# Kernel tuning notes

Hardware: AMD Instinct MI355X
Metric: run time of the kernel (lower is better)

## Reference

```python
import jax, jax.numpy as jnp
import numpy as np

N, Fdim, Aout = 8192, 32, 8
AVG_DEG = 32.0  # target average degree for the random graph


def setup_inputs() -> dict:
    key = jax.random.key(0)
    ks = jax.random.split(key, 12)
    x = jax.random.normal(ks[0], (N, Fdim), dtype=jnp.float32)
    # binary adjacency, zero diagonal (GCNConv adds self-loops itself)
    u = jax.random.uniform(ks[1], (N, N), dtype=jnp.float32)
    adj = (u < (AVG_DEG / N)).astype(jnp.float32)
    adj = adj * (1.0 - jnp.eye(N, dtype=jnp.float32))
    mask = (jax.random.uniform(ks[2], (N,), dtype=jnp.float32) < 0.5).astype(jnp.float32)

    def lin(k, fout, fin):
        s = 1.0 / np.sqrt(fin)
        return jax.random.uniform(k, (fout, fin), jnp.float32, -s, s)

    return {
        "x": x, "adj": adj, "mask": mask,
        "w1": lin(ks[3], 64, Fdim), "b1": jnp.zeros((64,), jnp.float32),
        "w2": lin(ks[4], 128, 64), "b2": jnp.zeros((128,), jnp.float32),
        "wg": lin(ks[5], 128, 128), "bg": jnp.zeros((128,), jnp.float32),
        "wd": lin(ks[6], 128, 128), "bd": jnp.zeros((128,), jnp.float32),
        "wp1": lin(ks[7], 128, 256), "bp1": jnp.zeros((128,), jnp.float32),
        "wp2": lin(ks[8], 64, 128), "bp2": jnp.zeros((64,), jnp.float32),
        "wo": lin(ks[9], Aout, 64), "bo": jnp.zeros((Aout,), jnp.float32),
    }


def reference(x, adj, mask, w1, b1, w2, b2, wg, bg, wd, bd, wp1, bp1, wp2, bp2, wo, bo):
    # encoder MLP
    h = jax.nn.relu(x @ w1.T + b1)           # [N,64]
    h = jax.nn.relu(h @ w2.T + b2)           # [N,128]
    # GCNConv with default self-loops and symmetric normalization:
    # out = D^{-1/2} (A + I) D^{-1/2} (h W^T) + b
    a_hat = adj + jnp.eye(adj.shape[0], dtype=adj.dtype)
    deg = jnp.sum(a_hat, axis=1)             # >= 1 thanks to self-loops
    dinv = jax.lax.rsqrt(deg)
    msg = h @ wg.T                            # [N,128]
    agg = dinv[:, None] * (a_hat @ (dinv[:, None] * msg))  # normalized aggregation
    g = jax.nn.relu(agg + bg)
    g = jax.nn.relu(g @ wd.T + bd)
    f = jnp.concatenate([g, h], axis=1)       # [N,256]
    p = jax.nn.relu(f @ wp1.T + bp1)
    p = jax.nn.relu(p @ wp2.T + bp2)
    out = (p @ wo.T + bo) * mask[:, None]     # [N,Aout]
    return out
```

## Files before the change

kernel.cpp:

```cpp
#include <hip/hip_runtime.h>

#define N_NODES 8192
#define CAP 128
#define ETILE 16
#define DTILE 8
constexpr int AST = 132;
constexpr int WST = 129;

typedef unsigned u32x4 __attribute__((ext_vector_type(4)));

__global__ __launch_bounds__(256, 4) void scan_kernel(
    const float* __restrict__ adj, int* __restrict__ cnt,
    int* __restrict__ nbr) {
  const int t = threadIdx.x;
  const int lane = t & 63;
  const int row = blockIdx.x * 4 + (t >> 6);
  const u32x4* rowp = (const u32x4*)(adj + (size_t)row * N_NODES);
  u32x4 v[8], vn[8];
#pragma unroll
  for (int i = 0; i < 8; ++i) v[i] = __builtin_nontemporal_load(&rowp[i * 64 + lane]);
  int running = 0;
  int* nbr_row = nbr + (size_t)row * CAP;
  for (int ch = 0; ch < 4; ++ch) {
    if (ch < 3) {
      const u32x4* cp = rowp + (ch + 1) * 512;
#pragma unroll
      for (int i = 0; i < 8; ++i) vn[i] = __builtin_nontemporal_load(&cp[i * 64 + lane]);
    }
    int c = 0;
#pragma unroll
    for (int i = 0; i < 8; ++i)
      c += (v[i].x != 0u) + (v[i].y != 0u) + (v[i].z != 0u) + (v[i].w != 0u);
    int incl = c;
#pragma unroll
    for (int s = 1; s < 64; s <<= 1) {
      int n = __shfl_up(incl, s);
      if (lane >= s) incl += n;
    }
    int off = running + incl - c;
    running += __shfl(incl, 63);
    const int colbase = ch * 2048;
#pragma unroll
    for (int i = 0; i < 8; ++i) {
      if (v[i].x | v[i].y | v[i].z | v[i].w) {
        const int col = colbase + (i * 64 + lane) * 4;
        if (v[i].x) { if (off < CAP) nbr_row[off] = col + 0; ++off; }
        if (v[i].y) { if (off < CAP) nbr_row[off] = col + 1; ++off; }
        if (v[i].z) { if (off < CAP) nbr_row[off] = col + 2; ++off; }
        if (v[i].w) { if (off < CAP) nbr_row[off] = col + 3; ++off; }
      }
    }
#pragma unroll
    for (int i = 0; i < 8; ++i) v[i] = vn[i];
  }
  if (lane == 0) cnt[row] = running;
}

template <int TILE, int K, int KSPLIT, int F, bool RELU, bool BIAS, int SCALEMODE>
__device__ __forceinline__ void layer_op(
    const float (*__restrict__ A0)[AST], const float (*__restrict__ A1)[AST],
    float (*__restrict__ Aout)[AST], float (*__restrict__ Wb)[WST],
    const float* __restrict__ W, const float* __restrict__ bias,
    float* __restrict__ gout, const float* __restrict__ rowscale,
    const int* __restrict__ degcnt, int n0, int t) {
  constexpr int KC = 32;
  constexpr int NCH = K / KC;
  constexpr int ACT = (F * TILE < 256) ? F * TILE : 256;
  constexpr int RS = ACT / F;
  constexpr int RPT = TILE / RS;
  const int c = t % F;
  const int rb = t / F;
  float acc[RPT];
#pragma unroll
  for (int i = 0; i < RPT; ++i) acc[i] = 0.f;

  for (int ch = 0; ch < NCH; ++ch) {
#pragma unroll
    for (int i = 0; i < (F * KC + 255) / 256; ++i) {
      int lin = t + i * 256;
      if ((F * KC) % 256 == 0 || lin < F * KC) {
        int k = lin % KC, f = lin / KC;
        Wb[k][f] = W[(size_t)f * K + ch * KC + k];
      }
    }
    __syncthreads();
    if (t < ACT) {
      const float (*__restrict__ As)[AST] = (ch * KC < KSPLIT) ? A0 : A1;
      const int kb = (ch * KC < KSPLIT) ? ch * KC : ch * KC - KSPLIT;
#pragma unroll
      for (int kg = 0; kg < KC / 4; ++kg) {
        float w0 = Wb[kg * 4 + 0][c];
        float w1v = Wb[kg * 4 + 1][c];
        float w2v = Wb[kg * 4 + 2][c];
        float w3v = Wb[kg * 4 + 3][c];
#pragma unroll
        for (int i = 0; i < RPT; ++i) {
          const float4 a = *(const float4*)&As[rb + i * RS][kb + kg * 4];
          acc[i] = fmaf(a.x, w0, acc[i]);
          acc[i] = fmaf(a.y, w1v, acc[i]);
          acc[i] = fmaf(a.z, w2v, acc[i]);
          acc[i] = fmaf(a.w, w3v, acc[i]);
        }
      }
    }
    __syncthreads();
  }
  if (t < ACT) {
#pragma unroll
    for (int i = 0; i < RPT; ++i) {
      float v = acc[i];
      if (BIAS) v += bias[c];
      if (RELU) v = fmaxf(v, 0.f);
      int node = n0 + rb + i * RS;
      if (SCALEMODE == 1) v *= rowscale[node];
      if (SCALEMODE == 2) v *= rsqrtf((float)degcnt[node] + 1.0f);
      if (Aout) Aout[rb + i * RS][c] = v;
      if (gout) gout[(size_t)node * F + c] = v;
    }
  }
}

__global__ __launch_bounds__(256) void encode_kernel(
    const float* __restrict__ x,
    const float* __restrict__ w1, const float* __restrict__ b1,
    const float* __restrict__ w2, const float* __restrict__ b2,
    const float* __restrict__ wg, const int* __restrict__ cnt,
    float* __restrict__ h_out, float* __restrict__ msg_out) {
  __shared__ float bufA[ETILE][AST];
  __shared__ float bufB[ETILE][AST];
  __shared__ float Wb[32][WST];
  const int t = threadIdx.x;
  const int n0 = blockIdx.x * ETILE;
  if (t < 128) {
    int row = t >> 3, k4 = (t & 7) * 4;
    *(float4*)&bufA[row][k4] = *(const float4*)&x[(size_t)(n0 + row) * 32 + k4];
  }
  layer_op<ETILE, 32, 32, 64, true, true, 0>(bufA, nullptr, bufB, Wb, w1, b1, nullptr, nullptr, nullptr, n0, t);
  layer_op<ETILE, 64, 64, 128, true, true, 0>(bufB, nullptr, bufA, Wb, w2, b2, h_out, nullptr, nullptr, n0, t);
  layer_op<ETILE, 128, 128, 128, false, false, 2>(bufA, nullptr, nullptr, Wb, wg, nullptr, msg_out, nullptr, cnt, n0, t);
}

__global__ __launch_bounds__(256) void agg_kernel(
    const int* __restrict__ cnt, const int* __restrict__ nbr,
    const float* __restrict__ msg, const float* __restrict__ bg,
    const float* __restrict__ adj, float* __restrict__ g1) {
  const int t = threadIdx.x;
  const int f = t & 127;
  const int rA = blockIdx.x * 4 + (t >> 7) * 2;
  const int rB = rA + 1;
  const int cA = cnt[rA], cB = cnt[rB];
  float a0 = msg[(size_t)rA * 128 + f];
  float a1 = msg[(size_t)rB * 128 + f];
  if (cA <= CAP && cB <= CAP) {
    const int* nA = nbr + (size_t)rA * CAP;
    const int* nB = nbr + (size_t)rB * CAP;
    const int cm = max(cA, cB);
    for (int i = 0; i < cm; i += 4) {
#pragma unroll
      for (int k = 0; k < 4; ++k) {
        const int ii = i + k;
        int jA = nA[ii < cA ? ii : 0] & (N_NODES - 1);
        int jB = nB[ii < cB ? ii : 0] & (N_NODES - 1);
        float vA = msg[(size_t)jA * 128 + f];
        float vB = msg[(size_t)jB * 128 + f];
        a0 += (ii < cA) ? vA : 0.f;
        a1 += (ii < cB) ? vB : 0.f;
      }
    }
  } else {
    a0 = msg[(size_t)rA * 128 + f];
    a1 = msg[(size_t)rB * 128 + f];
    for (int col = 0; col < N_NODES; ++col) {
      if (adj[(size_t)rA * N_NODES + col] != 0.f) a0 += msg[(size_t)col * 128 + f];
      if (adj[(size_t)rB * N_NODES + col] != 0.f) a1 += msg[(size_t)col * 128 + f];
    }
  }
  float o0 = fmaf(rsqrtf((float)cA + 1.0f), a0, bg[f]);
  float o1 = fmaf(rsqrtf((float)cB + 1.0f), a1, bg[f]);
  g1[(size_t)rA * 128 + f] = fmaxf(o0, 0.f);
  g1[(size_t)rB * 128 + f] = fmaxf(o1, 0.f);
}

__global__ __launch_bounds__(256) void decode_kernel(
    const float* __restrict__ g1, const float* __restrict__ h,
    const float* __restrict__ wd, const float* __restrict__ bd,
    const float* __restrict__ wp1, const float* __restrict__ bp1,
    const float* __restrict__ wp2, const float* __restrict__ bp2,
    const float* __restrict__ wo, const float* __restrict__ bo,
    const float* __restrict__ mask, float* __restrict__ out) {
  __shared__ float bufA[DTILE][AST];
  __shared__ float bufB[DTILE][AST];
  __shared__ float bufH[DTILE][AST];
  __shared__ float Wb[32][WST];
  const int t = threadIdx.x;
  const int n0 = blockIdx.x * DTILE;
  {
    int row = t >> 5, k4 = (t & 31) * 4;
    *(float4*)&bufA[row][k4] = *(const float4*)&g1[(size_t)(n0 + row) * 128 + k4];
    *(float4*)&bufH[row][k4] = *(const float4*)&h[(size_t)(n0 + row) * 128 + k4];
  }
  layer_op<DTILE, 128, 128, 128, true, true, 0>(bufA, nullptr, bufB, Wb, wd, bd, nullptr, nullptr, nullptr, n0, t);
  layer_op<DTILE, 256, 128, 128, true, true, 0>(bufB, bufH, bufA, Wb, wp1, bp1, nullptr, nullptr, nullptr, n0, t);
  layer_op<DTILE, 128, 128, 64, true, true, 0>(bufA, nullptr, bufB, Wb, wp2, bp2, nullptr, nullptr, nullptr, n0, t);
  layer_op<DTILE, 64, 64, 8, false, true, 1>(bufB, nullptr, nullptr, Wb, wo, bo, out, mask, nullptr, n0, t);
}

extern "C" void kernel_launch(void* const* d_in, const int* in_sizes, int n_in,
                              void* d_out, int out_size, void* d_ws, size_t ws_size,
                              hipStream_t stream) {
  const float* x    = (const float*)d_in[0];
  const float* adj  = (const float*)d_in[1];
  const float* mask = (const float*)d_in[2];
  const float* w1   = (const float*)d_in[3];
  const float* b1   = (const float*)d_in[4];
  const float* w2   = (const float*)d_in[5];
  const float* b2   = (const float*)d_in[6];
  const float* wg   = (const float*)d_in[7];
  const float* bg   = (const float*)d_in[8];
  const float* wd   = (const float*)d_in[9];
  const float* bd   = (const float*)d_in[10];
  const float* wp1  = (const float*)d_in[11];
  const float* bp1  = (const float*)d_in[12];
  const float* wp2  = (const float*)d_in[13];
  const float* bp2  = (const float*)d_in[14];
  const float* wo   = (const float*)d_in[15];
  const float* bo   = (const float*)d_in[16];
  float* out = (float*)d_out;

  float* ws = (float*)d_ws;
  float* h    = ws; ws += (size_t)N_NODES * 128;
  float* msg  = ws; ws += (size_t)N_NODES * 128;
  float* g1   = ws; ws += (size_t)N_NODES * 128;
  int* cnt = (int*)ws; ws += N_NODES;
  int* nbr = (int*)ws;

  scan_kernel<<<N_NODES / 4, 256, 0, stream>>>(adj, cnt, nbr);
  encode_kernel<<<N_NODES / ETILE, 256, 0, stream>>>(x, w1, b1, w2, b2, wg, cnt, h, msg);
  agg_kernel<<<N_NODES / 4, 256, 0, stream>>>(cnt, nbr, msg, bg, adj, g1);
  decode_kernel<<<N_NODES / DTILE, 256, 0, stream>>>(
      g1, h, wd, bd, wp1, bp1, wp2, bp2, wo, bo, mask, out);
}
```

Baseline: 455.3 us.

## Use 2D register-tiled GEMM with 32-row tiles in encode/decode MLP kernels

```diff
diff --git a/kernel.cpp b/kernel.cpp
--- a/kernel.cpp
+++ b/kernel.cpp
@@ -2,10 +2,9 @@
 
 #define N_NODES 8192
 #define CAP 128
-#define ETILE 16
-#define DTILE 8
+#define MT 32
 constexpr int AST = 132;
-constexpr int WST = 129;
+constexpr int WST = 132;
 
 typedef unsigned u32x4 __attribute__((ext_vector_type(4)));
 
@@ -16,11 +15,11 @@
   const int lane = t & 63;
   const int row = blockIdx.x * 4 + (t >> 6);
   const u32x4* rowp = (const u32x4*)(adj + (size_t)row * N_NODES);
+  int* nbr_row = nbr + (size_t)row * CAP;
   u32x4 v[8], vn[8];
 #pragma unroll
   for (int i = 0; i < 8; ++i) v[i] = __builtin_nontemporal_load(&rowp[i * 64 + lane]);
   int running = 0;
-  int* nbr_row = nbr + (size_t)row * CAP;
   for (int ch = 0; ch < 4; ++ch) {
     if (ch < 3) {
       const u32x4* cp = rowp + (ch + 1) * 512;
@@ -56,8 +55,8 @@
   if (lane == 0) cnt[row] = running;
 }
 
-template <int TILE, int K, int KSPLIT, int F, bool RELU, bool BIAS, int SCALEMODE>
-__device__ __forceinline__ void layer_op(
+template <int K, int KSPLIT, int F, bool RELU, bool BIAS, int SCALEMODE>
+__device__ __forceinline__ void layer2d(
     const float (*__restrict__ A0)[AST], const float (*__restrict__ A1)[AST],
     float (*__restrict__ Aout)[AST], float (*__restrict__ Wb)[WST],
     const float* __restrict__ W, const float* __restrict__ bias,
@@ -65,58 +64,72 @@
     const int* __restrict__ degcnt, int n0, int t) {
   constexpr int KC = 32;
   constexpr int NCH = K / KC;
-  constexpr int ACT = (F * TILE < 256) ? F * TILE : 256;
-  constexpr int RS = ACT / F;
-  constexpr int RPT = TILE / RS;
-  const int c = t % F;
-  const int rb = t / F;
-  float acc[RPT];
-#pragma unroll
-  for (int i = 0; i < RPT; ++i) acc[i] = 0.f;
+  constexpr int WC = (F >= 128) ? 2 : 1;
+  constexpr int WR = 4 / WC;
+  constexpr int TC = F / WC / 16;
+  constexpr int TR = MT / WR / 4;
+  const int w = t >> 6, lane = t & 63;
+  const int wc = w % WC, wr = w / WC;
+  const int cg = lane & 15, rg = lane >> 4;
+  const int c0 = wc * (F / WC) + cg * TC;
+  const int r0 = wr * (MT / WR) + rg * TR;
+  float acc[TR][TC] = {};
 
   for (int ch = 0; ch < NCH; ++ch) {
 #pragma unroll
-    for (int i = 0; i < (F * KC + 255) / 256; ++i) {
+    for (int i = 0; i < (F * KC) / 256; ++i) {
       int lin = t + i * 256;
-      if ((F * KC) % 256 == 0 || lin < F * KC) {
-        int k = lin % KC, f = lin / KC;
-        Wb[k][f] = W[(size_t)f * K + ch * KC + k];
-      }
+      int k = lin % KC, f = lin / KC;
+      Wb[k][f] = W[(size_t)f * K + ch * KC + k];
     }
     __syncthreads();
-    if (t < ACT) {
-      const float (*__restrict__ As)[AST] = (ch * KC < KSPLIT) ? A0 : A1;
-      const int kb = (ch * KC < KSPLIT) ? ch * KC : ch * KC - KSPLIT;
-#pragma unroll
-      for (int kg = 0; kg < KC / 4; ++kg) {
-        float w0 = Wb[kg * 4 + 0][c];
-        float w1v = Wb[kg * 4 + 1][c];
-        float w2v = Wb[kg * 4 + 2][c];
-        float w3v = Wb[kg * 4 + 3][c];
-#pragma unroll
-        for (int i = 0; i < RPT; ++i) {
-          const float4 a = *(const float4*)&As[rb + i * RS][kb + kg * 4];
-          acc[i] = fmaf(a.x, w0, acc[i]);
-          acc[i] = fmaf(a.y, w1v, acc[i]);
-          acc[i] = fmaf(a.z, w2v, acc[i]);
-          acc[i] = fmaf(a.w, w3v, acc[i]);
+    const float (*__restrict__ As)[AST] = (ch * KC < KSPLIT) ? A0 : A1;
+    const int kb = (ch * KC < KSPLIT) ? ch * KC : ch * KC - KSPLIT;
+#pragma unroll
+    for (int kg = 0; kg < KC / 4; ++kg) {
+      float4 a[TR], wv[4];
+#pragma unroll
+      for (int i = 0; i < TR; ++i)
+        a[i] = *(const float4*)&As[r0 + i][kb + kg * 4];
+#pragma unroll
+      for (int kk = 0; kk < 4; ++kk)
+        wv[kk] = *(const float4*)&Wb[kg * 4 + kk][c0];
+#pragma unroll
+      for (int i = 0; i < TR; ++i) {
+#pragma unroll
+        for (int j = 0; j < TC; ++j) {
+          float* ap = (float*)&a[i];
+          float s = acc[i][j];
+          s = fmaf(ap[0], ((const float*)&wv[0])[j], s);
+          s = fmaf(ap[1], ((const float*)&wv[1])[j], s);
+          s = fmaf(ap[2], ((const float*)&wv[2])[j], s);
+          s = fmaf(ap[3], ((const float*)&wv[3])[j], s);
+          acc[i][j] = s;
         }
       }
     }
     __syncthreads();
   }
-  if (t < ACT) {
-#pragma unroll
-    for (int i = 0; i < RPT; ++i) {
-      float v = acc[i];
-      if (BIAS) v += bias[c];
+  float4 bv = make_float4(0.f, 0.f, 0.f, 0.f);
+  if (BIAS) bv = *(const float4*)&bias[c0];
+#pragma unroll
+  for (int i = 0; i < TR; ++i) {
+    const int node = n0 + r0 + i;
+    float scale = 1.f;
+    if (SCALEMODE == 1) scale = rowscale[node];
+    if (SCALEMODE == 2) scale = rsqrtf((float)degcnt[node] + 1.0f);
+    float4 o;
+    float* op = (float*)&o;
+#pragma unroll
+    for (int j = 0; j < TC; ++j) {
+      float v = acc[i][j];
+      if (BIAS) v += ((const float*)&bv)[j];
       if (RELU) v = fmaxf(v, 0.f);
-      int node = n0 + rb + i * RS;
-      if (SCALEMODE == 1) v *= rowscale[node];
-      if (SCALEMODE == 2) v *= rsqrtf((float)degcnt[node] + 1.0f);
-      if (Aout) Aout[rb + i * RS][c] = v;
-      if (gout) gout[(size_t)node * F + c] = v;
-    }
+      if (SCALEMODE) v *= scale;
+      op[j] = v;
+    }
+    if (Aout) *(float4*)&Aout[r0 + i][c0] = o;
+    if (gout) *(float4*)&gout[(size_t)node * F + c0] = o;
   }
 }
 
@@ -126,18 +139,18 @@
     const float* __restrict__ w2, const float* __restrict__ b2,
     const float* __restrict__ wg, const int* __restrict__ cnt,
     float* __restrict__ h_out, float* __restrict__ msg_out) {
-  __shared__ float bufA[ETILE][AST];
-  __shared__ float bufB[ETILE][AST];
+  __shared__ float bufA[MT][AST];
+  __shared__ float bufB[MT][AST];
   __shared__ float Wb[32][WST];
   const int t = threadIdx.x;
-  const int n0 = blockIdx.x * ETILE;
-  if (t < 128) {
+  const int n0 = blockIdx.x * MT;
+  {
     int row = t >> 3, k4 = (t & 7) * 4;
     *(float4*)&bufA[row][k4] = *(const float4*)&x[(size_t)(n0 + row) * 32 + k4];
   }
-  layer_op<ETILE, 32, 32, 64, true, true, 0>(bufA, nullptr, bufB, Wb, w1, b1, nullptr, nullptr, nullptr, n0, t);
-  layer_op<ETILE, 64, 64, 128, true, true, 0>(bufB, nullptr, bufA, Wb, w2, b2, h_out, nullptr, nullptr, n0, t);
-  layer_op<ETILE, 128, 128, 128, false, false, 2>(bufA, nullptr, nullptr, Wb, wg, nullptr, msg_out, nullptr, cnt, n0, t);
+  layer2d<32, 32, 64, true, true, 0>(bufA, nullptr, bufB, Wb, w1, b1, nullptr, nullptr, nullptr, n0, t);
+  layer2d<64, 64, 128, true, true, 0>(bufB, nullptr, bufA, Wb, w2, b2, h_out, nullptr, nullptr, n0, t);
+  layer2d<128, 128, 128, false, false, 2>(bufA, nullptr, nullptr, Wb, wg, nullptr, msg_out, nullptr, cnt, n0, t);
 }
 
 __global__ __launch_bounds__(256) void agg_kernel(
@@ -188,21 +201,39 @@
     const float* __restrict__ wp2, const float* __restrict__ bp2,
     const float* __restrict__ wo, const float* __restrict__ bo,
     const float* __restrict__ mask, float* __restrict__ out) {
-  __shared__ float bufA[DTILE][AST];
-  __shared__ float bufB[DTILE][AST];
-  __shared__ float bufH[DTILE][AST];
+  __shared__ float bufA[MT][AST];
+  __shared__ float bufB[MT][AST];
+  __shared__ float bufH[MT][AST];
   __shared__ float Wb[32][WST];
   const int t = threadIdx.x;
-  const int n0 = blockIdx.x * DTILE;
-  {
-    int row = t >> 5, k4 = (t & 31) * 4;
+  const int n0 = blockIdx.x * MT;
+#pragma unroll
+  for (int i = 0; i < 4; ++i) {
+    int lin = t + i * 256;
+    int row = lin >> 5, k4 = (lin & 31) * 4;
     *(float4*)&bufA[row][k4] = *(const float4*)&g1[(size_t)(n0 + row) * 128 + k4];
     *(float4*)&bufH[row][k4] = *(const float4*)&h[(size_t)(n0 + row) * 128 + k4];
   }
-  layer_op<DTILE, 128, 128, 128, true, true, 0>(bufA, nullptr, bufB, Wb, wd, bd, nullptr, nullptr, nullptr, n0, t);
-  layer_op<DTILE, 256, 128, 128, true, true, 0>(bufB, bufH, bufA, Wb, wp1, bp1, nullptr, nullptr, nullptr, n0, t);
-  layer_op<DTILE, 128, 128, 64, true, true, 0>(bufA, nullptr, bufB, Wb, wp2, bp2, nullptr, nullptr, nullptr, n0, t);
-  layer_op<DTILE, 64, 64, 8, false, true, 1>(bufB, nullptr, nullptr, Wb, wo, bo, out, mask, nullptr, n0, t);
+  layer2d<128, 128, 128, true, true, 0>(bufA, nullptr, bufB, Wb, wd, bd, nullptr, nullptr, nullptr, n0, t);
+  layer2d<256, 128, 128, true, true, 0>(bufB, bufH, bufA, Wb, wp1, bp1, nullptr, nullptr, nullptr, n0, t);
+  layer2d<128, 128, 64, true, true, 0>(bufA, nullptr, bufB, Wb, wp2, bp2, nullptr, nullptr, nullptr, n0, t);
+  __syncthreads();
+  {
+    const int row = t >> 3, c = t & 7;
+    const float* wrow = wo + c * 64;
+    float accv = 0.f;
+#pragma unroll
+    for (int k4 = 0; k4 < 16; ++k4) {
+      float4 a = *(const float4*)&bufB[row][k4 * 4];
+      float4 wv = *(const float4*)&wrow[k4 * 4];
+      accv = fmaf(a.x, wv.x, accv);
+      accv = fmaf(a.y, wv.y, accv);
+      accv = fmaf(a.z, wv.z, accv);
+      accv = fmaf(a.w, wv.w, accv);
+    }
+    const int node = n0 + row;
+    out[(size_t)node * 8 + c] = (accv + bo[c]) * mask[node];
+  }
 }
 
 extern "C" void kernel_launch(void* const* d_in, const int* in_sizes, int n_in,
@@ -235,8 +266,8 @@
   int* nbr = (int*)ws;
 
   scan_kernel<<<N_NODES / 4, 256, 0, stream>>>(adj, cnt, nbr);
-  encode_kernel<<<N_NODES / ETILE, 256, 0, stream>>>(x, w1, b1, w2, b2, wg, cnt, h, msg);
+  encode_kernel<<<N_NODES / MT, 256, 0, stream>>>(x, w1, b1, w2, b2, wg, cnt, h, msg);
   agg_kernel<<<N_NODES / 4, 256, 0, stream>>>(cnt, nbr, msg, bg, adj, g1);
-  decode_kernel<<<N_NODES / DTILE, 256, 0, stream>>>(
+  decode_kernel<<<N_NODES / MT, 256, 0, stream>>>(
       g1, h, wd, bd, wp1, bp1, wp2, bp2, wo, bo, mask, out);
 }
```

After: 484.7 us. +6.5%, slower.
